# Kernel tuning notes

Measured on AMD Instinct MI355X. Metric: run time of the kernel, lower is better.

Reference implementation:

```python
import jax, jax.numpy as jnp
import numpy as np

GROUP_SIZE = 128
IN_FEATURES = 4096
OUT_FEATURES = 11008
MAX_INT = 16  # 2**w_bit with w_bit=4


def setup_inputs() -> dict:
    key = jax.random.key(0)
    k0, k1, k2, k3, k4 = jax.random.split(key, 5)
    n_grp = IN_FEATURES // GROUP_SIZE
    x = jax.random.normal(k0, (1, 32, IN_FEATURES), dtype=jnp.float32)
    # qweight stored transposed as [in, out], values in [0, 2^w_bit - 1]
    qweight = jax.random.randint(k1, (IN_FEATURES, OUT_FEATURES), 0, MAX_INT, dtype=jnp.int32)
    qzeros = jax.random.randint(k2, (n_grp, OUT_FEATURES), 0, MAX_INT, dtype=jnp.int32)
    scales = jax.random.uniform(k3, (n_grp, OUT_FEATURES), dtype=jnp.float32) * 0.01
    bias = jax.random.normal(k4, (OUT_FEATURES,), dtype=jnp.float32)
    return {"x": x, "qweight": qweight, "qzeros": qzeros, "scales": scales, "bias": bias}


def reference(x, qweight, qzeros, scales, bias):
    # Per-group dequantize: w[g*G+j, o] = (qw - qz[g,o]) * sc[g,o]
    n_grp = qweight.shape[0] // GROUP_SIZE
    qw = qweight.reshape(n_grp, GROUP_SIZE, -1).astype(jnp.float32)  # [n_grp, G, out]
    # scales are stored as bfloat16 in the torch module
    sc = scales.astype(jnp.bfloat16).astype(jnp.float32)
    w = (qw - qzeros[:, None, :].astype(jnp.float32)) * sc[:, None, :]
    w = w.reshape(qweight.shape[0], qweight.shape[1])  # [in, out]
    # forward_cpu: x -> bf16 -> f32, then matmul + bias
    xf = x.astype(jnp.bfloat16).astype(jnp.float32)
    bf = bias.astype(jnp.bfloat16).astype(jnp.float32)
    return jnp.einsum('bsi,io->bso', xf, w) + bf
```

## Files before the change

### kernel.cpp

```cpp
#include <hip/hip_runtime.h>
#include <hip/hip_bf16.h>

#define IN_F   4096
#define OUT_F  11008
#define GS     128
#define NGRP   32
#define M      32
#define TILE_N 512
#define NT     22

__device__ __forceinline__ float bf16r(float v) {
    return __bfloat162float(__float2bfloat16(v));
}

__global__ __launch_bounds__(256) void qk_main(
    const float* __restrict__ x, const int* __restrict__ qw,
    const int* __restrict__ qz, const float* __restrict__ sc,
    __hip_bfloat16* __restrict__ part)
{
    const int g  = blockIdx.y;
    const int tx = threadIdx.x;

    __shared__ float xs[GS][M];
    #pragma unroll
    for (int i = tx; i < GS * M; i += 256) {
        int m  = i & (M - 1);
        int kk = i >> 5;
        xs[kk][m] = bf16r(x[m * IN_F + g * GS + kk]);
    }

    int n0  = blockIdx.x * TILE_N + tx * 2;
    int n0c = n0 > OUT_F - 2 ? OUT_F - 2 : n0;

    const float2 scv = *(const float2*)(sc + (size_t)g * OUT_F + n0c);
    const int2   qzv = *(const int2*)  (qz + (size_t)g * OUT_F + n0c);
    float s0 = bf16r(scv.x), s1 = bf16r(scv.y);
    float o0 = -(float)qzv.x * s0;
    float o1 = -(float)qzv.y * s1;

    float acc0[M], acc1[M];
    #pragma unroll
    for (int m = 0; m < M; ++m) { acc0[m] = 0.f; acc1[m] = 0.f; }

    const int* qp = qw + (size_t)g * GS * OUT_F + n0c;

    __syncthreads();

    #pragma unroll 8
    for (int kk = 0; kk < GS; ++kk) {
        int2 q = *(const int2*)qp;
        qp += OUT_F;
        float w0 = (float)q.x * s0 + o0;
        float w1 = (float)q.y * s1 + o1;
        const float4* xv = (const float4*)&xs[kk][0];
        #pragma unroll
        for (int j = 0; j < M / 4; ++j) {
            float4 xx = xv[j];
            acc0[4*j+0] += xx.x * w0;  acc1[4*j+0] += xx.x * w1;
            acc0[4*j+1] += xx.y * w0;  acc1[4*j+1] += xx.y * w1;
            acc0[4*j+2] += xx.z * w0;  acc1[4*j+2] += xx.z * w1;
            acc0[4*j+3] += xx.w * w0;  acc1[4*j+3] += xx.w * w1;
        }
    }

    if (n0 < OUT_F) {
        __hip_bfloat16* pp = part + (size_t)g * M * OUT_F + n0;
        #pragma unroll
        for (int m = 0; m < M; ++m) {
            __hip_bfloat162 hv;
            hv.x = __float2bfloat16(acc0[m]);
            hv.y = __float2bfloat16(acc1[m]);
            *(__hip_bfloat162*)(pp + (size_t)m * OUT_F) = hv;
        }
    }
}

__global__ __launch_bounds__(256) void qk_red(
    const __hip_bfloat16* __restrict__ part,
    const float* __restrict__ bias, float* __restrict__ out)
{
    const int m  = blockIdx.y;
    const int n0 = (blockIdx.x * 256 + threadIdx.x) * 2;
    if (n0 >= OUT_F) return;
    float a0 = 0.f, a1 = 0.f;
    #pragma unroll
    for (int gi = 0; gi < NGRP; ++gi) {
        __hip_bfloat162 v = *(const __hip_bfloat162*)(
            part + ((size_t)gi * M + m) * OUT_F + n0);
        a0 += __bfloat162float(v.x);
        a1 += __bfloat162float(v.y);
    }
    float2 r;
    r.x = a0 + bf16r(bias[n0]);
    r.y = a1 + bf16r(bias[n0 + 1]);
    *(float2*)(out + (size_t)m * OUT_F + n0) = r;
}

extern "C" void kernel_launch(void* const* d_in, const int* in_sizes, int n_in,
                              void* d_out, int out_size, void* d_ws, size_t ws_size,
                              hipStream_t stream) {
    const float* x    = (const float*)d_in[0];
    const int*   qw   = (const int*)  d_in[1];
    const int*   qz   = (const int*)  d_in[2];
    const float* sc   = (const float*)d_in[3];
    const float* bias = (const float*)d_in[4];
    float* out = (float*)d_out;
    __hip_bfloat16* part = (__hip_bfloat16*)d_ws;

    dim3 g1(NT, NGRP, 1);
    qk_main<<<g1, dim3(256, 1, 1), 0, stream>>>(x, qw, qz, sc, part);

    dim3 g2((OUT_F / 2 + 255) / 256, M, 1);
    qk_red<<<g2, dim3(256, 1, 1), 0, stream>>>(part, bias, out);
}
```

Before: 281.0 us.

## Double K chunk per block and software-pipeline qweight loads into registers

Each block now covers two quantization groups (256 rows of K), so the grid shrinks from 32 to 16 K-splits and the partial buffer and reduction pass get half as large. The inner loop is restructured to double-buffer int2 weight loads in register arrays of 8 rows. The next 8 rows are prefetched while the current 8 are dequantized and accumulated, hiding global load latency. The cost is fewer blocks (352 versus 704), which lowers parallelism on a large GPU, plus higher register pressure from the extra buffers.

```diff
diff --git a/kernel.cpp b/kernel.cpp
--- a/kernel.cpp
+++ b/kernel.cpp
@@ -4,8 +4,9 @@
 #define IN_F   4096
 #define OUT_F  11008
 #define GS     128
-#define NGRP   32
 #define M      32
+#define KCH    256
+#define NSPLIT 16
 #define TILE_N 512
 #define NT     22
 
@@ -18,53 +19,99 @@
     const int* __restrict__ qz, const float* __restrict__ sc,
     __hip_bfloat16* __restrict__ part)
 {
-    const int g  = blockIdx.y;
+    const int ks = blockIdx.y;
     const int tx = threadIdx.x;
 
-    __shared__ float xs[GS][M];
+    __shared__ float xs[KCH][M];
     #pragma unroll
-    for (int i = tx; i < GS * M; i += 256) {
+    for (int i = tx; i < KCH * M; i += 256) {
         int m  = i & (M - 1);
         int kk = i >> 5;
-        xs[kk][m] = bf16r(x[m * IN_F + g * GS + kk]);
+        xs[kk][m] = bf16r(x[m * IN_F + ks * KCH + kk]);
     }
 
     int n0  = blockIdx.x * TILE_N + tx * 2;
     int n0c = n0 > OUT_F - 2 ? OUT_F - 2 : n0;
 
-    const float2 scv = *(const float2*)(sc + (size_t)g * OUT_F + n0c);
-    const int2   qzv = *(const int2*)  (qz + (size_t)g * OUT_F + n0c);
-    float s0 = bf16r(scv.x), s1 = bf16r(scv.y);
-    float o0 = -(float)qzv.x * s0;
-    float o1 = -(float)qzv.y * s1;
+    const int g0 = ks * 2;
+    float2 sa = *(const float2*)(sc + (size_t)g0       * OUT_F + n0c);
+    float2 sb = *(const float2*)(sc + (size_t)(g0 + 1) * OUT_F + n0c);
+    int2   za = *(const int2*)  (qz + (size_t)g0       * OUT_F + n0c);
+    int2   zb = *(const int2*)  (qz + (size_t)(g0 + 1) * OUT_F + n0c);
+    float s0a = bf16r(sa.x), s1a = bf16r(sa.y);
+    float s0b = bf16r(sb.x), s1b = bf16r(sb.y);
+    float o0a = -(float)za.x * s0a, o1a = -(float)za.y * s1a;
+    float o0b = -(float)zb.x * s0b, o1b = -(float)zb.y * s1b;
 
     float acc0[M], acc1[M];
     #pragma unroll
     for (int m = 0; m < M; ++m) { acc0[m] = 0.f; acc1[m] = 0.f; }
 
-    const int* qp = qw + (size_t)g * GS * OUT_F + n0c;
+    const int* qbase = qw + (size_t)ks * KCH * OUT_F + n0c;
+
+    int2 qA[8], qB[8];
+    #pragma unroll
+    for (int j = 0; j < 8; ++j)
+        qA[j] = *(const int2*)(qbase + (size_t)j * OUT_F);
 
     __syncthreads();
 
-    #pragma unroll 8
-    for (int kk = 0; kk < GS; ++kk) {
-        int2 q = *(const int2*)qp;
-        qp += OUT_F;
-        float w0 = (float)q.x * s0 + o0;
-        float w1 = (float)q.y * s1 + o1;
-        const float4* xv = (const float4*)&xs[kk][0];
+    for (int c = 0; c < 16; ++c) {
+        float cs0 = c < 8 ? s0a : s0b;
+        float cs1 = c < 8 ? s1a : s1b;
+        float co0 = c < 8 ? o0a : o0b;
+        float co1 = c < 8 ? o1a : o1b;
+
+        int rB = (2 * c + 1) * 8;
         #pragma unroll
-        for (int j = 0; j < M / 4; ++j) {
-            float4 xx = xv[j];
-            acc0[4*j+0] += xx.x * w0;  acc1[4*j+0] += xx.x * w1;
-            acc0[4*j+1] += xx.y * w0;  acc1[4*j+1] += xx.y * w1;
-            acc0[4*j+2] += xx.z * w0;  acc1[4*j+2] += xx.z * w1;
-            acc0[4*j+3] += xx.w * w0;  acc1[4*j+3] += xx.w * w1;
+        for (int j = 0; j < 8; ++j)
+            qB[j] = *(const int2*)(qbase + (size_t)(rB + j) * OUT_F);
+
+        {
+            int kb = 16 * c;
+            #pragma unroll
+            for (int j = 0; j < 8; ++j) {
+                float w0 = (float)qA[j].x * cs0 + co0;
+                float w1 = (float)qA[j].y * cs1 + co1;
+                const float4* xv = (const float4*)&xs[kb + j][0];
+                #pragma unroll
+                for (int q4 = 0; q4 < M / 4; ++q4) {
+                    float4 xx = xv[q4];
+                    acc0[4*q4+0] += xx.x * w0;  acc1[4*q4+0] += xx.x * w1;
+                    acc0[4*q4+1] += xx.y * w0;  acc1[4*q4+1] += xx.y * w1;
+                    acc0[4*q4+2] += xx.z * w0;  acc1[4*q4+2] += xx.z * w1;
+                    acc0[4*q4+3] += xx.w * w0;  acc1[4*q4+3] += xx.w * w1;
+                }
+            }
+        }
+
+        int rA = (2 * c + 2) * 8;
+        if (rA > KCH - 8) rA = KCH - 8;
+        #pragma unroll
+        for (int j = 0; j < 8; ++j)
+            qA[j] = *(const int2*)(qbase + (size_t)(rA + j) * OUT_F);
+
+        {
+            int kb = 16 * c + 8;
+            #pragma unroll
+            for (int j = 0; j < 8; ++j) {
+                float w0 = (float)qB[j].x * cs0 + co0;
+                float w1 = (float)qB[j].y * cs1 + co1;
+                const float4* xv = (const float4*)&xs[kb + j][0];
+                #pragma unroll
+                for (int q4 = 0; q4 < M / 4; ++q4) {
+                    float4 xx = xv[q4];
+                    acc0[4*q4+0] += xx.x * w0;  acc1[4*q4+0] += xx.x * w1;
+                    acc0[4*q4+1] += xx.y * w0;  acc1[4*q4+1] += xx.y * w1;
+                    acc0[4*q4+2] += xx.z * w0;  acc1[4*q4+2] += xx.z * w1;
+                    acc0[4*q4+3] += xx.w * w0;  acc1[4*q4+3] += xx.w * w1;
+                }
+            }
         }
     }
 
     if (n0 < OUT_F) {
-        __hip_bfloat16* pp = part + (size_t)g * M * OUT_F + n0;
+        __hip_bfloat16* pp = part + (size_t)ks * M * OUT_F + n0;
         #pragma unroll
         for (int m = 0; m < M; ++m) {
             __hip_bfloat162 hv;
@@ -84,9 +131,9 @@
     if (n0 >= OUT_F) return;
     float a0 = 0.f, a1 = 0.f;
     #pragma unroll
-    for (int gi = 0; gi < NGRP; ++gi) {
+    for (int s = 0; s < NSPLIT; ++s) {
         __hip_bfloat162 v = *(const __hip_bfloat162*)(
-            part + ((size_t)gi * M + m) * OUT_F + n0);
+            part + ((size_t)s * M + m) * OUT_F + n0);
         a0 += __bfloat162float(v.x);
         a1 += __bfloat162float(v.y);
     }
@@ -107,7 +154,7 @@
     float* out = (float*)d_out;
     __hip_bfloat16* part = (__hip_bfloat16*)d_ws;
 
-    dim3 g1(NT, NGRP, 1);
+    dim3 g1(NT, NSPLIT, 1);
     qk_main<<<g1, dim3(256, 1, 1), 0, stream>>>(x, qw, qz, sc, part);
 
     dim3 g2((OUT_F / 2 + 255) / 256, M, 1);
```

Result: no change. 280.9 us (-0.0%).
